# Optimization experiments

Measured on AMD Instinct MI355X. Metric: run time of the kernel, lower is better.

Reference implementation:

```python
import jax, jax.numpy as jnp
import numpy as np

FIX_SIGMA = (1.0, 2.0, 4.0, 8.0, 16.0)


def setup_inputs() -> dict:
    key = jax.random.key(0)
    k1, k2 = jax.random.split(key)
    B, C, D = 512, 32, 512
    source = jax.random.normal(k1, (B, C, D), dtype=jnp.float32)
    target = jax.random.normal(k2, (B, C, D), dtype=jnp.float32)
    return {"source": source, "target": target}


def _mmd(source, target):
    B = source.shape[0]
    total = jnp.concatenate([source, target], axis=0)  # [N, C, D], N = 2B
    # Pairwise per-channel squared L2 distance via norm expansion
    # (mathematically identical to ((x_i - x_j)**2).sum(-1), no [N,N,C,D] intermediate)
    sq = jnp.sum(total * total, axis=-1)  # [N, C]
    cross = jnp.einsum("icd,jcd->ijc", total, total)  # [N, N, C]
    L2 = sq[:, None, :] + sq[None, :, :] - 2.0 * cross  # [N, N, C]
    kernels = sum(jnp.exp(-L2 / sigma) for sigma in FIX_SIGMA)  # [N, N, C]
    XX = kernels[:B, :B, :]
    YY = kernels[B:, B:, :]
    XY = kernels[:B, B:, :]
    YX = kernels[B:, :B, :]
    loss_1 = XX + YY - XY - YX  # [B, B, C]
    # mean over dim0, mean over dim0 again (i.e. both batch dims), sum over channels
    return jnp.sum(jnp.mean(loss_1, axis=(0, 1)))


def reference(source, target):
    return _mmd(source, target)
```

## Files before the change

kernel.cpp:

```cpp
#include <hip/hip_runtime.h>

namespace {

constexpr int kC = 32;
constexpr int kD = 512;
constexpr int kB = 512;
constexpr int kN = 1024;
constexpr int kCD = kC * kD;
constexpr int BM = 128;
constexpr int BK = 32;
constexpr int KSTEPS = kD / BK;
constexpr int TILES = kN / BM;
constexpr int NPAIRS = TILES * (TILES + 1) / 2;

typedef float f32x4 __attribute__((ext_vector_type(4)));
typedef short s16x8 __attribute__((ext_vector_type(8)));

__device__ inline unsigned int pack_bf16(float a, float b) {
  unsigned int ua = __float_as_uint(a);
  unsigned int ub = __float_as_uint(b);
  ua += 0x7fffu + ((ua >> 16) & 1u);
  ub += 0x7fffu + ((ub >> 16) & 1u);
  return (ua >> 16) | (ub & 0xffff0000u);
}

__global__ void prep_kernel(const float* __restrict__ src,
                            const float* __restrict__ tgt,
                            float* __restrict__ sq,
                            unsigned int* __restrict__ tot,
                            float* __restrict__ out) {
  if (blockIdx.x == 0 && threadIdx.x == 0) *out = 0.f;
  int gw = (blockIdx.x * blockDim.x + threadIdx.x) >> 6;
  int lane = threadIdx.x & 63;
  int i = gw >> 5;
  int c = gw & 31;
  const float* p = (i < kB ? src + (size_t)i * kCD
                           : tgt + (size_t)(i - kB) * kCD) + c * kD;
  f32x4 v0 = *(const f32x4*)(p + lane * 8);
  f32x4 v1 = *(const f32x4*)(p + lane * 8 + 4);

  uint4 w = make_uint4(pack_bf16(v0.x, v0.y), pack_bf16(v0.z, v0.w),
                       pack_bf16(v1.x, v1.y), pack_bf16(v1.z, v1.w));
  *(uint4*)(tot + (size_t)(c * kN + i) * (kD / 2) + lane * 4) = w;

  float s = v0.x * v0.x + v0.y * v0.y + v0.z * v0.z + v0.w * v0.w
          + v1.x * v1.x + v1.y * v1.y + v1.z * v1.z + v1.w * v1.w;
#pragma unroll
  for (int o = 32; o > 0; o >>= 1) s += __shfl_down(s, o);
  if (lane == 0) sq[c * kN + i] = s;
}

__launch_bounds__(256, 3)
__global__ void mmd_kernel(const unsigned short* __restrict__ tot,
                           const float* __restrict__ sq,
                           float* __restrict__ out) {
  int b = blockIdx.x;
  int c = b & 31;
  int p = b >> 5;
  int ti = 0;
  while (p >= TILES - ti) { p -= TILES - ti; ++ti; }
  int tj = ti + p;

  __shared__ __align__(16) unsigned short lA[3][BM * BK];
  __shared__ __align__(16) unsigned short lB[3][BM * BK];
  __shared__ float wsum[4];

  const int t = threadIdx.x;
  const int lane = t & 63;
  const int wid = t >> 6;
  const int wr = wid >> 1;
  const int wc = wid & 1;

  const unsigned short* gA = tot + (size_t)(c * kN + ti * BM) * kD;
  const unsigned short* gB = tot + (size_t)(c * kN + tj * BM) * kD;

  const int srow = ((lane >> 3) << 1) + ((lane >> 2) & 1);
  const int scch = (lane & 3) ^ ((lane >> 3) & 3);

  auto STAGE = [&](int buf, int ks) {
#pragma unroll
    for (int q = 0; q < 2; ++q) {
      int i = wid * 2 + q;
      int r = 16 * i + srow;
      const unsigned short* sa = gA + (size_t)r * kD + ks * BK + scch * 8;
      const unsigned short* sb = gB + (size_t)r * kD + ks * BK + scch * 8;
      __builtin_amdgcn_global_load_lds(
          (const __attribute__((address_space(1))) unsigned int*)sa,
          (__attribute__((address_space(3))) unsigned int*)&lA[buf][i * 512],
          16, 0, 0);
      __builtin_amdgcn_global_load_lds(
          (const __attribute__((address_space(1))) unsigned int*)sb,
          (__attribute__((address_space(3))) unsigned int*)&lB[buf][i * 512],
          16, 0, 0);
    }
  };

  const int l15 = lane & 15;
  const int s4 = lane >> 4;
  const int laneoff = ((l15 >> 1) << 7) + ((l15 & 1) << 6) +
                      ((s4 ^ ((l15 >> 1) & 3)) << 4);

  f32x4 acc[4][4] = {};

  STAGE(0, 0);
  STAGE(1, 1);

#pragma unroll
  for (int ks = 0; ks < KSTEPS; ++ks) {
    if (ks + 1 < KSTEPS) asm volatile("s_waitcnt vmcnt(4)" ::: "memory");
    else                 asm volatile("s_waitcnt vmcnt(0)" ::: "memory");
    __builtin_amdgcn_sched_barrier(0);
    __builtin_amdgcn_s_barrier();

    const int buf = ks % 3;
    const char* Abase = (const char*)lA[buf] + wr * 4096 + laneoff;
    const char* Bbase = (const char*)lB[buf] + wc * 4096 + laneoff;
    s16x8 aF[4], bF[4];
#pragma unroll
    for (int m = 0; m < 4; ++m) aF[m] = *(const s16x8*)(Abase + m * 1024);
#pragma unroll
    for (int n = 0; n < 4; ++n) bF[n] = *(const s16x8*)(Bbase + n * 1024);

    if (ks + 2 < KSTEPS) STAGE((ks + 2) % 3, ks + 2);

    __builtin_amdgcn_s_setprio(1);
#pragma unroll
    for (int m = 0; m < 4; ++m)
#pragma unroll
      for (int n = 0; n < 4; ++n)
        acc[m][n] = __builtin_amdgcn_mfma_f32_16x16x32_bf16(
            aF[m], bF[n], acc[m][n], 0, 0, 0);
    __builtin_amdgcn_s_setprio(0);
  }

  const float sA = (ti < TILES / 2) ? 1.f : -1.f;
  const float sB = (tj < TILES / 2) ? 1.f : -1.f;
  const float scale = sA * sB * ((ti == tj) ? 1.f : 2.f) / 262144.f;
  const float* sqA = sq + c * kN + ti * BM;
  const float* sqB = sq + c * kN + tj * BM;

  float local = 0.f;
#pragma unroll
  for (int m = 0; m < 4; ++m) {
    float sqa_r[4];
#pragma unroll
    for (int rI = 0; rI < 4; ++rI)
      sqa_r[rI] = sqA[wr * 64 + m * 16 + (lane >> 4) * 4 + rI];
#pragma unroll
    for (int n = 0; n < 4; ++n) {
      float sqb_ = sqB[wc * 64 + n * 16 + (lane & 15)];
#pragma unroll
      for (int rI = 0; rI < 4; ++rI) {
        float L2 = sqa_r[rI] + sqb_ - 2.f * acc[m][n][rI];
        float tt = __expf(L2 * -0.0625f);
        float t2 = tt * tt, t4 = t2 * t2, t8 = t4 * t4;
        local += tt + t2 + t4 + t8 + t8 * t8;
      }
    }
  }

#pragma unroll
  for (int o = 32; o > 0; o >>= 1) local += __shfl_down(local, o);
  if (lane == 0) wsum[wid] = local;
  __syncthreads();
  if (t == 0)
    atomicAdd(out, (wsum[0] + wsum[1] + wsum[2] + wsum[3]) * scale);
}

}

extern "C" void kernel_launch(void* const* d_in, const int* in_sizes, int n_in,
                              void* d_out, int out_size, void* d_ws,
                              size_t ws_size, hipStream_t stream) {
  const float* src = (const float*)d_in[0];
  const float* tgt = (const float*)d_in[1];
  float* out = (float*)d_out;

  float* sq = (float*)d_ws;
  unsigned int* tot = (unsigned int*)((char*)d_ws + (size_t)kC * kN * 4);

  {
    int blocks = (kN * kC) / 4;
    prep_kernel<<<blocks, 256, 0, stream>>>(src, tgt, sq, tot, out);
  }
  {
    mmd_kernel<<<NPAIRS * kC, 256, 0, stream>>>((const unsigned short*)tot, sq, out);
  }
}
```

Before: 52.24 us.

## Enlarge tile to 256 with 8 waves and split A/B staging per half-step

Tile size goes from 128 to 256 rows, with 512-thread blocks of 8 waves, each computing a 128x64 sub-tile (8x4 MFMA accumulators). This halves the number of tile pairs and cuts the global/LDS traffic per FLOP. The K loop now runs in two phases, each with its own A or B staging call and extra barriers and lgkmcnt waits, to overlap loads with MFMA. The costs are more register pressure, fewer blocks (320) for the GPU's CUs, and more barriers per k-step.

Measured after the change: 62.88 us. 20.4% more time.

```diff
diff --git a/kernel.cpp b/kernel.cpp
--- a/kernel.cpp
+++ b/kernel.cpp
@@ -7,11 +7,11 @@
 constexpr int kB = 512;
 constexpr int kN = 1024;
 constexpr int kCD = kC * kD;
-constexpr int BM = 128;
-constexpr int BK = 32;
-constexpr int KSTEPS = kD / BK;
-constexpr int TILES = kN / BM;
-constexpr int NPAIRS = TILES * (TILES + 1) / 2;
+constexpr int BM = 256;
+constexpr int BKt = 32;
+constexpr int KT = kD / BKt;
+constexpr int T2 = kN / BM;
+constexpr int NP = T2 * (T2 + 1) / 2;
 
 typedef float f32x4 __attribute__((ext_vector_type(4)));
 typedef short s16x8 __attribute__((ext_vector_type(8)));
@@ -50,26 +50,26 @@
   if (lane == 0) sq[c * kN + i] = s;
 }
 
-__launch_bounds__(256, 3)
+__launch_bounds__(512, 2)
 __global__ void mmd_kernel(const unsigned short* __restrict__ tot,
                            const float* __restrict__ sq,
                            float* __restrict__ out) {
-  int b = blockIdx.x;
-  int c = b & 31;
+  const int b = blockIdx.x;
+  const int c = b & 31;
   int p = b >> 5;
   int ti = 0;
-  while (p >= TILES - ti) { p -= TILES - ti; ++ti; }
+  while (p >= T2 - ti) { p -= T2 - ti; ++ti; }
   int tj = ti + p;
 
-  __shared__ __align__(16) unsigned short lA[3][BM * BK];
-  __shared__ __align__(16) unsigned short lB[3][BM * BK];
-  __shared__ float wsum[4];
+  __shared__ __align__(16) unsigned short lA[3][BM * BKt];
+  __shared__ __align__(16) unsigned short lB[3][BM * BKt];
+  __shared__ float wsum[8];
 
   const int t = threadIdx.x;
   const int lane = t & 63;
   const int wid = t >> 6;
-  const int wr = wid >> 1;
-  const int wc = wid & 1;
+  const int wr = wid >> 2;
+  const int wcn = wid & 3;
 
   const unsigned short* gA = tot + (size_t)(c * kN + ti * BM) * kD;
   const unsigned short* gB = tot + (size_t)(c * kN + tj * BM) * kD;
@@ -77,19 +77,26 @@
   const int srow = ((lane >> 3) << 1) + ((lane >> 2) & 1);
   const int scch = (lane & 3) ^ ((lane >> 3) & 3);
 
-  auto STAGE = [&](int buf, int ks) {
+  auto STAGE_A = [&](int buf, int kt) {
 #pragma unroll
     for (int q = 0; q < 2; ++q) {
       int i = wid * 2 + q;
       int r = 16 * i + srow;
-      const unsigned short* sa = gA + (size_t)r * kD + ks * BK + scch * 8;
-      const unsigned short* sb = gB + (size_t)r * kD + ks * BK + scch * 8;
+      const unsigned short* s = gA + (size_t)r * kD + kt * BKt + scch * 8;
       __builtin_amdgcn_global_load_lds(
-          (const __attribute__((address_space(1))) unsigned int*)sa,
+          (const __attribute__((address_space(1))) unsigned int*)s,
           (__attribute__((address_space(3))) unsigned int*)&lA[buf][i * 512],
           16, 0, 0);
+    }
+  };
+  auto STAGE_B = [&](int buf, int kt) {
+#pragma unroll
+    for (int q = 0; q < 2; ++q) {
+      int i = wid * 2 + q;
+      int r = 16 * i + srow;
+      const unsigned short* s = gB + (size_t)r * kD + kt * BKt + scch * 8;
       __builtin_amdgcn_global_load_lds(
-          (const __attribute__((address_space(1))) unsigned int*)sb,
+          (const __attribute__((address_space(1))) unsigned int*)s,
           (__attribute__((address_space(3))) unsigned int*)&lB[buf][i * 512],
           16, 0, 0);
     }
@@ -100,29 +107,30 @@
   const int laneoff = ((l15 >> 1) << 7) + ((l15 & 1) << 6) +
                       ((s4 ^ ((l15 >> 1) & 3)) << 4);
 
-  f32x4 acc[4][4] = {};
-
-  STAGE(0, 0);
-  STAGE(1, 1);
-
-#pragma unroll
-  for (int ks = 0; ks < KSTEPS; ++ks) {
-    if (ks + 1 < KSTEPS) asm volatile("s_waitcnt vmcnt(4)" ::: "memory");
-    else                 asm volatile("s_waitcnt vmcnt(0)" ::: "memory");
-    __builtin_amdgcn_sched_barrier(0);
-    __builtin_amdgcn_s_barrier();
-
-    const int buf = ks % 3;
-    const char* Abase = (const char*)lA[buf] + wr * 4096 + laneoff;
-    const char* Bbase = (const char*)lB[buf] + wc * 4096 + laneoff;
+  f32x4 acc[8][4] = {};
+
+  STAGE_A(0, 0); STAGE_B(0, 0);
+  STAGE_A(1, 1); STAGE_B(1, 1);
+  asm volatile("s_waitcnt vmcnt(4)" ::: "memory");
+  __builtin_amdgcn_sched_barrier(0);
+  __builtin_amdgcn_s_barrier();
+
+#pragma unroll
+  for (int kt = 0; kt < KT; ++kt) {
+    const int buf = kt % 3;
+    const char* Abase = (const char*)lA[buf] + wr * 8192 + laneoff;
+    const char* Bbase = (const char*)lB[buf] + wcn * 4096 + laneoff;
+
     s16x8 aF[4], bF[4];
 #pragma unroll
     for (int m = 0; m < 4; ++m) aF[m] = *(const s16x8*)(Abase + m * 1024);
 #pragma unroll
     for (int n = 0; n < 4; ++n) bF[n] = *(const s16x8*)(Bbase + n * 1024);
-
-    if (ks + 2 < KSTEPS) STAGE((ks + 2) % 3, ks + 2);
-
+    if (kt + 2 < KT) STAGE_A((kt + 2) % 3, kt + 2);
+    __builtin_amdgcn_sched_barrier(0);
+    __builtin_amdgcn_s_barrier();
+    asm volatile("s_waitcnt lgkmcnt(0)" ::: "memory");
+    __builtin_amdgcn_sched_barrier(0);
     __builtin_amdgcn_s_setprio(1);
 #pragma unroll
     for (int m = 0; m < 4; ++m)
@@ -131,24 +139,48 @@
         acc[m][n] = __builtin_amdgcn_mfma_f32_16x16x32_bf16(
             aF[m], bF[n], acc[m][n], 0, 0, 0);
     __builtin_amdgcn_s_setprio(0);
-  }
-
-  const float sA = (ti < TILES / 2) ? 1.f : -1.f;
-  const float sB = (tj < TILES / 2) ? 1.f : -1.f;
+    __builtin_amdgcn_sched_barrier(0);
+    __builtin_amdgcn_s_barrier();
+
+#pragma unroll
+    for (int m = 0; m < 4; ++m)
+      aF[m] = *(const s16x8*)(Abase + (m + 4) * 1024);
+    if (kt + 2 < KT) STAGE_B((kt + 2) % 3, kt + 2);
+    __builtin_amdgcn_sched_barrier(0);
+    __builtin_amdgcn_s_barrier();
+    asm volatile("s_waitcnt lgkmcnt(0)" ::: "memory");
+    __builtin_amdgcn_sched_barrier(0);
+    __builtin_amdgcn_s_setprio(1);
+#pragma unroll
+    for (int m = 0; m < 4; ++m)
+#pragma unroll
+      for (int n = 0; n < 4; ++n)
+        acc[m + 4][n] = __builtin_amdgcn_mfma_f32_16x16x32_bf16(
+            aF[m], bF[n], acc[m + 4][n], 0, 0, 0);
+    __builtin_amdgcn_s_setprio(0);
+
+    if (kt < KT - 2) asm volatile("s_waitcnt vmcnt(4)" ::: "memory");
+    else if (kt == KT - 2) asm volatile("s_waitcnt vmcnt(0)" ::: "memory");
+    __builtin_amdgcn_sched_barrier(0);
+    __builtin_amdgcn_s_barrier();
+  }
+
+  const float sA = (ti < T2 / 2) ? 1.f : -1.f;
+  const float sB = (tj < T2 / 2) ? 1.f : -1.f;
   const float scale = sA * sB * ((ti == tj) ? 1.f : 2.f) / 262144.f;
-  const float* sqA = sq + c * kN + ti * BM;
-  const float* sqB = sq + c * kN + tj * BM;
+  const float* sqA = sq + c * kN + ti * BM + wr * 128;
+  const float* sqB = sq + c * kN + tj * BM + wcn * 64;
 
   float local = 0.f;
 #pragma unroll
-  for (int m = 0; m < 4; ++m) {
+  for (int m = 0; m < 8; ++m) {
     float sqa_r[4];
 #pragma unroll
     for (int rI = 0; rI < 4; ++rI)
-      sqa_r[rI] = sqA[wr * 64 + m * 16 + (lane >> 4) * 4 + rI];
+      sqa_r[rI] = sqA[m * 16 + (lane >> 4) * 4 + rI];
 #pragma unroll
     for (int n = 0; n < 4; ++n) {
-      float sqb_ = sqB[wc * 64 + n * 16 + (lane & 15)];
+      float sqb_ = sqB[n * 16 + (lane & 15)];
 #pragma unroll
       for (int rI = 0; rI < 4; ++rI) {
         float L2 = sqa_r[rI] + sqb_ - 2.f * acc[m][n][rI];
@@ -158,13 +190,18 @@
       }
     }
   }
+  local *= scale;
 
 #pragma unroll
   for (int o = 32; o > 0; o >>= 1) local += __shfl_down(local, o);
   if (lane == 0) wsum[wid] = local;
   __syncthreads();
-  if (t == 0)
-    atomicAdd(out, (wsum[0] + wsum[1] + wsum[2] + wsum[3]) * scale);
+  if (t == 0) {
+    float s = 0.f;
+#pragma unroll
+    for (int w = 0; w < 8; ++w) s += wsum[w];
+    atomicAdd(out, s);
+  }
 }
 
 }
@@ -184,6 +221,7 @@
     prep_kernel<<<blocks, 256, 0, stream>>>(src, tgt, sq, tot, out);
   }
   {
-    mmd_kernel<<<NPAIRS * kC, 256, 0, stream>>>((const unsigned short*)tot, sq, out);
-  }
-}
+    int blocks = NP * kC;
+    mmd_kernel<<<blocks, 512, 0, stream>>>((const unsigned short*)tot, sq, out);
+  }
+}
```

## Share A tile across two B tiles per block with 512-thread workgroups

Applied to the files above, without the earlier changes.

Each block now handles one row tile against two column tiles (paired via constant lookup tables), so the A tile is loaded once and reused by two 4-wave groups, cutting global/LDS traffic for A. Block count drops from 36 to 20 per channel, and the diagonal self-pair is weighted by 0.5 to avoid double counting. Per-block scaling is applied before the wave reduction. The trade-off is larger LDS per block, fewer blocks, and possible load imbalance, with occupancy set to 2 blocks of 512 threads.

Measured after the change: 55.41 us. 1.06x slower.

```diff
diff --git a/kernel.cpp b/kernel.cpp
--- a/kernel.cpp
+++ b/kernel.cpp
@@ -8,13 +8,16 @@
 constexpr int kN = 1024;
 constexpr int kCD = kC * kD;
 constexpr int BM = 128;
-constexpr int BK = 32;
-constexpr int KSTEPS = kD / BK;
-constexpr int TILES = kN / BM;
-constexpr int NPAIRS = TILES * (TILES + 1) / 2;
+constexpr int BKt = 32;
+constexpr int KT = kD / BKt;
+constexpr int NG = 20;
 
 typedef float f32x4 __attribute__((ext_vector_type(4)));
 typedef short s16x8 __attribute__((ext_vector_type(8)));
+
+__device__ __constant__ int gTi[NG] = {0,0,0,0, 1,1,1,1, 2,2,2, 3,3,3, 4,4, 5,5, 6, 7};
+__device__ __constant__ int gT0[NG] = {0,2,4,6, 1,3,5,7, 2,4,6, 3,5,7, 4,6, 5,7, 6, 7};
+__device__ __constant__ int gT1[NG] = {1,3,5,7, 2,4,6,7, 3,5,7, 4,6,7, 5,7, 6,7, 7, 7};
 
 __device__ inline unsigned int pack_bf16(float a, float b) {
   unsigned int ua = __float_as_uint(a);
@@ -50,49 +53,50 @@
   if (lane == 0) sq[c * kN + i] = s;
 }
 
-__launch_bounds__(256, 3)
+__launch_bounds__(512, 2)
 __global__ void mmd_kernel(const unsigned short* __restrict__ tot,
                            const float* __restrict__ sq,
                            float* __restrict__ out) {
-  int b = blockIdx.x;
-  int c = b & 31;
-  int p = b >> 5;
-  int ti = 0;
-  while (p >= TILES - ti) { p -= TILES - ti; ++ti; }
-  int tj = ti + p;
-
-  __shared__ __align__(16) unsigned short lA[3][BM * BK];
-  __shared__ __align__(16) unsigned short lB[3][BM * BK];
-  __shared__ float wsum[4];
+  const int b = blockIdx.x;
+  const int c = b & 31;
+  const int g = b >> 5;
+  const int ti = gTi[g];
+  const int t0 = gT0[g];
+  const int t1 = gT1[g];
+
+  __shared__ __align__(16) unsigned short lA[3][BM * BKt];
+  __shared__ __align__(16) unsigned short lB[3][2][BM * BKt];
+  __shared__ float wsum[8];
 
   const int t = threadIdx.x;
   const int lane = t & 63;
   const int wid = t >> 6;
-  const int wr = wid >> 1;
+  const int bsel = wid >> 2;
+  const int wr = (wid >> 1) & 1;
   const int wc = wid & 1;
 
-  const unsigned short* gA = tot + (size_t)(c * kN + ti * BM) * kD;
-  const unsigned short* gB = tot + (size_t)(c * kN + tj * BM) * kD;
+  const unsigned short* gA  = tot + (size_t)(c * kN + ti * BM) * kD;
+  const unsigned short* gB0 = tot + (size_t)(c * kN + t0 * BM) * kD;
+  const unsigned short* gB1 = tot + (size_t)(c * kN + t1 * BM) * kD;
 
   const int srow = ((lane >> 3) << 1) + ((lane >> 2) & 1);
   const int scch = (lane & 3) ^ ((lane >> 3) & 3);
 
   auto STAGE = [&](int buf, int ks) {
-#pragma unroll
-    for (int q = 0; q < 2; ++q) {
-      int i = wid * 2 + q;
-      int r = 16 * i + srow;
-      const unsigned short* sa = gA + (size_t)r * kD + ks * BK + scch * 8;
-      const unsigned short* sb = gB + (size_t)r * kD + ks * BK + scch * 8;
-      __builtin_amdgcn_global_load_lds(
-          (const __attribute__((address_space(1))) unsigned int*)sa,
-          (__attribute__((address_space(3))) unsigned int*)&lA[buf][i * 512],
-          16, 0, 0);
-      __builtin_amdgcn_global_load_lds(
-          (const __attribute__((address_space(1))) unsigned int*)sb,
-          (__attribute__((address_space(3))) unsigned int*)&lB[buf][i * 512],
-          16, 0, 0);
-    }
+    int r = 16 * wid + srow;
+    size_t off = (size_t)r * kD + ks * BKt + scch * 8;
+    __builtin_amdgcn_global_load_lds(
+        (const __attribute__((address_space(1))) unsigned int*)(gA + off),
+        (__attribute__((address_space(3))) unsigned int*)&lA[buf][wid * 512],
+        16, 0, 0);
+    __builtin_amdgcn_global_load_lds(
+        (const __attribute__((address_space(1))) unsigned int*)(gB0 + off),
+        (__attribute__((address_space(3))) unsigned int*)&lB[buf][0][wid * 512],
+        16, 0, 0);
+    __builtin_amdgcn_global_load_lds(
+        (const __attribute__((address_space(1))) unsigned int*)(gB1 + off),
+        (__attribute__((address_space(3))) unsigned int*)&lB[buf][1][wid * 512],
+        16, 0, 0);
   };
 
   const int l15 = lane & 15;
@@ -106,22 +110,22 @@
   STAGE(1, 1);
 
 #pragma unroll
-  for (int ks = 0; ks < KSTEPS; ++ks) {
-    if (ks + 1 < KSTEPS) asm volatile("s_waitcnt vmcnt(4)" ::: "memory");
-    else                 asm volatile("s_waitcnt vmcnt(0)" ::: "memory");
+  for (int ks = 0; ks < KT; ++ks) {
+    if (ks + 1 < KT) asm volatile("s_waitcnt vmcnt(3)" ::: "memory");
+    else             asm volatile("s_waitcnt vmcnt(0)" ::: "memory");
     __builtin_amdgcn_sched_barrier(0);
     __builtin_amdgcn_s_barrier();
 
     const int buf = ks % 3;
     const char* Abase = (const char*)lA[buf] + wr * 4096 + laneoff;
-    const char* Bbase = (const char*)lB[buf] + wc * 4096 + laneoff;
+    const char* Bbase = (const char*)lB[buf][bsel] + wc * 4096 + laneoff;
     s16x8 aF[4], bF[4];
 #pragma unroll
     for (int m = 0; m < 4; ++m) aF[m] = *(const s16x8*)(Abase + m * 1024);
 #pragma unroll
     for (int n = 0; n < 4; ++n) bF[n] = *(const s16x8*)(Bbase + n * 1024);
 
-    if (ks + 2 < KSTEPS) STAGE((ks + 2) % 3, ks + 2);
+    if (ks + 2 < KT) STAGE((ks + 2) % 3, ks + 2);
 
     __builtin_amdgcn_s_setprio(1);
 #pragma unroll
@@ -133,11 +137,12 @@
     __builtin_amdgcn_s_setprio(0);
   }
 
-  const float sA = (ti < TILES / 2) ? 1.f : -1.f;
-  const float sB = (tj < TILES / 2) ? 1.f : -1.f;
-  const float scale = sA * sB * ((ti == tj) ? 1.f : 2.f) / 262144.f;
-  const float* sqA = sq + c * kN + ti * BM;
-  const float* sqB = sq + c * kN + tj * BM;
+  const int tj = bsel ? t1 : t0;
+  const float sgn = ((ti < 4) == (tj < 4)) ? 1.f : -1.f;
+  const float wgt = ((ti == tj) ? 1.f : 2.f) * ((t0 == t1) ? 0.5f : 1.f);
+  const float scale = sgn * wgt / 262144.f;
+  const float* sqA = sq + c * kN + ti * BM + wr * 64;
+  const float* sqB = sq + c * kN + tj * BM + wc * 64;
 
   float local = 0.f;
 #pragma unroll
@@ -145,10 +150,10 @@
     float sqa_r[4];
 #pragma unroll
     for (int rI = 0; rI < 4; ++rI)
-      sqa_r[rI] = sqA[wr * 64 + m * 16 + (lane >> 4) * 4 + rI];
+      sqa_r[rI] = sqA[m * 16 + s4 * 4 + rI];
 #pragma unroll
     for (int n = 0; n < 4; ++n) {
-      float sqb_ = sqB[wc * 64 + n * 16 + (lane & 15)];
+      float sqb_ = sqB[n * 16 + l15];
 #pragma unroll
       for (int rI = 0; rI < 4; ++rI) {
         float L2 = sqa_r[rI] + sqb_ - 2.f * acc[m][n][rI];
@@ -158,13 +163,18 @@
       }
     }
   }
+  local *= scale;
 
 #pragma unroll
   for (int o = 32; o > 0; o >>= 1) local += __shfl_down(local, o);
   if (lane == 0) wsum[wid] = local;
   __syncthreads();
-  if (t == 0)
-    atomicAdd(out, (wsum[0] + wsum[1] + wsum[2] + wsum[3]) * scale);
+  if (t == 0) {
+    float s = 0.f;
+#pragma unroll
+    for (int w = 0; w < 8; ++w) s += wsum[w];
+    atomicAdd(out, s);
+  }
 }
 
 }
@@ -184,6 +194,7 @@
     prep_kernel<<<blocks, 256, 0, stream>>>(src, tgt, sq, tot, out);
   }
   {
-    mmd_kernel<<<NPAIRS * kC, 256, 0, stream>>>((const unsigned short*)tot, sq, out);
-  }
-}
+    int blocks = NG * kC;
+    mmd_kernel<<<blocks, 512, 0, stream>>>((const unsigned short*)tot, sq, out);
+  }
+}
```
